# Kernel optimization log

Measured on AMD Instinct MI355X. Metric: run time of the kernel, lower is better.

The kernel has to match this reference:

```python
import jax, jax.numpy as jnp
import numpy as np

B, T, C, H, D = 8, 2048, 1024, 1024, 4  # batch, seq_len, input_size, hidden_size, dilation


def setup_inputs() -> dict:
    key = jax.random.key(0)
    k1, k2, k3, k4, k5 = jax.random.split(key, 5)
    s = 1.0 / np.sqrt(H).astype(np.float32)  # match nn.LSTM uniform(-1/sqrt(H),1/sqrt(H)) scale
    return {
        "x": jax.random.normal(k1, (B, T, C), jnp.float32),
        "W_ih": jax.random.normal(k2, (4 * H, C), jnp.float32) * s,
        "W_hh": jax.random.normal(k3, (4 * H, H), jnp.float32) * s,
        "b_ih": jax.random.normal(k4, (4 * H,), jnp.float32) * s,
        "b_hh": jax.random.normal(k5, (4 * H,), jnp.float32) * s,
    }


def _dilated_lstm(x, W_ih, W_hh, b_ih, b_hh):
    Bv, Tv, Cv = x.shape
    Tp = -(-Tv // D) * D          # ceil(T/D)*D, static
    L = Tp // D                   # sub-sequence length per dilation phase
    xp = jnp.pad(x, ((0, 0), (0, Tp - Tv), (0, 0)))
    # (B, L, D, C) -> (B, D, L, C) -> (B*D, L, C): D parallel strided slices
    xr = xp.reshape(Bv, L, D, Cv).transpose(0, 2, 1, 3).reshape(Bv * D, L, Cv)
    # Precompute input contribution to all gates once (big GEMM, hoisted out of scan)
    xg = jnp.einsum('blc,gc->blg', xr, W_ih) + b_ih + b_hh  # (B*D, L, 4H)

    h0 = jnp.zeros((Bv * D, H), x.dtype)
    c0 = jnp.zeros((Bv * D, H), x.dtype)

    def step(carry, g_t):
        h, c = carry
        g = g_t + h @ W_hh.T                    # (B*D, 4H), torch gate order i,f,g,o
        i, f, gg, o = jnp.split(g, 4, axis=-1)
        i = jax.nn.sigmoid(i)
        f = jax.nn.sigmoid(f)
        gg = jnp.tanh(gg)
        o = jax.nn.sigmoid(o)
        c = f * c + i * gg
        h = o * jnp.tanh(c)
        return (h, c), h

    _, ys = jax.lax.scan(step, (h0, c0), xg.transpose(1, 0, 2))  # ys: (L, B*D, H)
    y = ys.transpose(1, 0, 2)                                    # (B*D, L, H)
    y = y.reshape(Bv, D, L, H).transpose(0, 2, 1, 3).reshape(Bv, Tp, H)
    return y[:, :Tv, :]


def reference(x, W_ih, W_hh, b_ih, b_hh):
    return _dilated_lstm(x, W_ih, W_hh, b_ih, b_hh)
```

## Files before the change

### kernel.cpp

```cpp
#include <hip/hip_runtime.h>
#include <cstdint>

typedef __attribute__((ext_vector_type(8))) _Float16 half8;
typedef __attribute__((ext_vector_type(4))) _Float16 half4;
typedef __attribute__((ext_vector_type(4))) float f32x4;
typedef unsigned short u16;
typedef unsigned int u32;
typedef unsigned long long u64;

#define MFMA16F(a, b, c) __builtin_amdgcn_mfma_f32_16x16x32_f16((a), (b), (c), 0, 0, 0)
#define AGENT __HIP_MEMORY_SCOPE_AGENT

template <int AUX>
__device__ __forceinline__ void gl_lds16_a(const void* g, void* lds) {
  __builtin_amdgcn_global_load_lds(
      (const __attribute__((address_space(1))) unsigned*)g,
      (__attribute__((address_space(3))) unsigned*)lds, 16, 0, AUX);
}

__device__ __forceinline__ float sigm(float x) { return 1.f / (1.f + __expf(-x)); }
__device__ __forceinline__ float tanh_f(float x) { return 2.f / (1.f + __expf(-2.f * x)) - 1.f; }

__global__ void k_cvt(const float* __restrict__ in, _Float16* __restrict__ o, int n4) {
  int i = blockIdx.x * blockDim.x + threadIdx.x;
  int stride = gridDim.x * blockDim.x;
  for (; i < n4; i += stride) {
    float4 v = ((const float4*)in)[i];
    half4 h = {(_Float16)v.x, (_Float16)v.y, (_Float16)v.z, (_Float16)v.w};
    ((half4*)o)[i] = h;
  }
}

__global__ void k_bias(const float* __restrict__ bi, const float* __restrict__ bh,
                       float* __restrict__ bias) {
  int i = blockIdx.x * blockDim.x + threadIdx.x;
  if (i < 4096) bias[i] = bi[i] + bh[i];
}

__global__ void k_init4(u64* __restrict__ hf, u32* __restrict__ rdz) {
  const int i = blockIdx.x * blockDim.x + threadIdx.x;
  const u64 v = (i < 8192) ? 0ull : 0x0001000100010001ull;
  __hip_atomic_store(&hf[i], v, __ATOMIC_RELAXED, AGENT);
  if (i < 16) __hip_atomic_store(&rdz[i], 0u, __ATOMIC_RELAXED, AGENT);
}

__global__ __launch_bounds__(256) void k_gemm1(
    const u16* __restrict__ Aw, const u16* __restrict__ Bw,
    const float* __restrict__ bias, _Float16* __restrict__ xg) {
  __shared__ u16 sA[4096];
  __shared__ u16 sB[4096];
  const int tid = threadIdx.x, lane = tid & 63, wid = tid >> 6;
  const int bm = blockIdx.x >> 5, bn = blockIdx.x & 31;
  const int m0 = bm * 128, n0 = bn * 128;
  const int wr = wid >> 1, wc = wid & 1;
  f32x4 acc[4][4] = {};

  for (int kt = 0; kt < 32; ++kt) {
#pragma unroll
    for (int rb = 0; rb < 2; ++rb) {
      const int base = (rb * 4 + wid) * 1024;
      const int b = base + lane * 16;
      const int row = b >> 6;
      const int q = lane & 3;
      const int sq = ((q - row) & 3) << 4;
      gl_lds16_a<0>((const char*)Aw + (size_t)(m0 + row) * 2048 + (size_t)kt * 64 + sq,
                    (char*)&sA[0] + base);
      gl_lds16_a<0>((const char*)Bw + (size_t)(n0 + row) * 2048 + (size_t)kt * 64 + sq,
                    (char*)&sB[0] + base);
    }
    __syncthreads();
    half8 ah[4], bh[4];
#pragma unroll
    for (int i = 0; i < 4; ++i) {
      const int ra = wr * 64 + i * 16 + (lane & 15);
      ah[i] = *(const half8*)((const char*)sA + ra * 64 + ((((lane >> 4) + ra) & 3) << 4));
      const int rb2 = wc * 64 + i * 16 + (lane & 15);
      bh[i] = *(const half8*)((const char*)sB + rb2 * 64 + ((((lane >> 4) + rb2) & 3) << 4));
    }
#pragma unroll
    for (int i = 0; i < 4; ++i)
#pragma unroll
      for (int j = 0; j < 4; ++j) acc[i][j] = MFMA16F(ah[i], bh[j], acc[i][j]);
    __syncthreads();
  }

#pragma unroll
  for (int j = 0; j < 4; ++j) {
    const int gcol = n0 + wc * 64 + j * 16 + (lane & 15);
    const int gate = gcol >> 10, jj = gcol & 1023;
    const float bv = bias[gcol];
#pragma unroll
    for (int i = 0; i < 4; ++i)
#pragma unroll
      for (int q = 0; q < 4; ++q) {
        const int m = m0 + wr * 64 + i * 16 + (lane >> 4) * 4 + q;
        const int b = m >> 11, t = m & 2047;
        const int s = (b << 2) | (t & 3);
        const int l = t >> 2;
        xg[(((size_t)(l * 32 + s)) * 1024 + jj) * 4 + gate] = (_Float16)(acc[i][j][q] + bv);
      }
  }
}

__global__ __launch_bounds__(512, 1) void k_scan(
    const u16* __restrict__ Whh16, const _Float16* __restrict__ xg,
    u16* __restrict__ hfrag, float* __restrict__ out, u32* __restrict__ rdz) {
  const int b = blockIdx.x;
  const int tid = threadIdx.x;
  const int lane = tid & 63, wid = tid >> 6;

  __shared__ u16 h_lds[2][4096];
  __shared__ u32 sh_gr, sh_wl, sh_mode;

  if (tid == 0) {
    u32 my;
    asm volatile("s_getreg_b32 %0, hwreg(HW_REG_XCC_ID)" : "=s"(my));
    my &= 7u;
    const u32 rank = __hip_atomic_fetch_add(&rdz[my], 1u, __ATOMIC_RELAXED, AGENT);
    __hip_atomic_fetch_add(&rdz[8], 1u, __ATOMIC_RELAXED, AGENT);
    while (__hip_atomic_load(&rdz[8], __ATOMIC_RELAXED, AGENT) < 256u)
      __builtin_amdgcn_s_sleep(1);
    u32 okloc = 1;
    for (int x = 0; x < 8; ++x)
      okloc &= (__hip_atomic_load(&rdz[x], __ATOMIC_RELAXED, AGENT) == 32u);
    sh_gr = okloc ? my : (u32)(b >> 5);
    sh_wl = okloc ? rank : (u32)(b & 31);
    sh_mode = okloc ? 0u : 1u;
  }
  __syncthreads();
  const int gr = (int)sh_gr, wl = (int)sh_wl;
  int mode = (int)sh_mode;
  const int j0 = wl * 32;

  half8 wf[32];
  {
    const int p = lane & 15;
    const int gate = p >> 2, c = p & 3;
    const int koff = (lane >> 4) * 8;
    const size_t rowbase = (size_t)(gate * 1024 + j0 + wid * 4 + c) * 1024;
#pragma unroll
    for (int ks = 0; ks < 32; ++ks) {
      wf[ks] = *(const half8*)(Whh16 + rowbase + ks * 32 + koff);
      asm volatile("" : "+v"(wf[ks]));
    }
  }

  const int m = (lane >> 2) & 3;
  const int jl = (wid << 2) | (lane & 3);
  const int s = gr * 4 + m;
  const int j = j0 + jl;
  float c_reg = 0.f;
  const int hq = wl * 32 + m * 8 + wid;

  const u64 M = 0x0001000100010001ull;

  float x0 = 0.f, x1 = 0.f, x2 = 0.f, x3 = 0.f;
  if (lane < 16) {
    const half4 xv = *(const half4*)(xg + ((size_t)s * 1024 + j) * 4);
    x0 = (float)xv[0]; x1 = (float)xv[1]; x2 = (float)xv[2]; x3 = (float)xv[3];
  }

  for (int l = 0; l < 512; ++l) {
    const char* hsrc = (const char*)hfrag + (size_t)(l & 3) * 65536 + gr * 8192;
    u64* hdst = (u64*)((char*)hfrag + (size_t)((l + 1) & 3) * 65536 + gr * 8192);
    const u64 expv = ((l >> 2) & 1) ? M : 0ull;
    const u32 pw = (u32)(((l + 1) >> 2) & 1);
    u16* ldsb = &h_lds[l & 1][0];

    {
      int tries = 0;
      for (;;) {
        if (mode == 0)
          gl_lds16_a<1>(hsrc + wid * 1024 + lane * 16, (char*)ldsb + wid * 1024);
        else
          gl_lds16_a<17>(hsrc + wid * 1024 + lane * 16, (char*)ldsb + wid * 1024);
        asm volatile("s_waitcnt vmcnt(0)" ::: "memory");
        const u64* q = (const u64*)((const char*)ldsb + wid * 1024 + lane * 16);
        const bool ok = (((q[0] ^ expv) & M) == 0) & (((q[1] ^ expv) & M) == 0);
        if (__all(ok)) break;
        if (++tries > 64) mode = 1;
      }
    }
    __syncthreads();

    f32x4 a0 = {0.f, 0.f, 0.f, 0.f}, a1 = a0, a2 = a0, a3 = a0;
    const char* ab = (const char*)ldsb + (lane & 3) * 64 + (lane >> 4) * 16;
#pragma unroll
    for (int ks = 0; ks < 32; ks += 4) {
      const char* cb = ab + ks * 256;
      a0 = MFMA16F(*(const half8*)(cb), wf[ks], a0);
      a1 = MFMA16F(*(const half8*)(cb + 256), wf[ks + 1], a1);
      a2 = MFMA16F(*(const half8*)(cb + 512), wf[ks + 2], a2);
      a3 = MFMA16F(*(const half8*)(cb + 768), wf[ks + 3], a3);
    }
    float G0 = (a0[0] + a1[0]) + (a2[0] + a3[0]);
    float G1 = (a0[1] + a1[1]) + (a2[1] + a3[1]);
    float G2 = (a0[2] + a1[2]) + (a2[2] + a3[2]);
    float G3 = (a0[3] + a1[3]) + (a2[3] + a3[3]);

    {
      const bool h2 = (lane & 4) != 0;
      float x, y;
      x = h2 ? G0 : G1; y = __shfl_xor(x, 4);
      G0 = h2 ? y : G0; G1 = h2 ? G1 : y;
      x = h2 ? G2 : G3; y = __shfl_xor(x, 4);
      G2 = h2 ? y : G2; G3 = h2 ? G3 : y;
    }
    {
      const bool h3 = (lane & 8) != 0;
      float x, y;
      x = h3 ? G0 : G2; y = __shfl_xor(x, 8);
      G0 = h3 ? y : G0; G2 = h3 ? G2 : y;
      x = h3 ? G1 : G3; y = __shfl_xor(x, 8);
      G1 = h3 ? y : G1; G3 = h3 ? G3 : y;
    }

    const float gi = G0 + x0, gf = G1 + x1, gg = G2 + x2, go = G3 + x3;
    const float iv = sigm(gi), fv = sigm(gf), gv = tanh_f(gg), ov = sigm(go);
    c_reg = fv * c_reg + iv * gv;
    const float hv = ov * tanh_f(c_reg);

    if (lane < 16) {
      u32 hb = (u32)__builtin_bit_cast(u16, (_Float16)hv);
      hb = (hb & 0xFFFEu) | pw;
      const u32 o1 = (u32)__shfl_xor((int)hb, 1);
      const u32 w1 = (lane & 1) ? ((o1 & 0xFFFFu) | (hb << 16))
                                : ((hb & 0xFFFFu) | (o1 << 16));
      const u32 o2lo = (u32)__shfl_xor((int)w1, 2);
      const u64 v = (lane & 2) ? (((u64)w1 << 32) | (u64)o2lo)
                               : (((u64)o2lo << 32) | (u64)w1);
      if ((lane & 3) == 0)
        __hip_atomic_store(&hdst[hq], v, __ATOMIC_RELAXED, AGENT);

      out[(((size_t)(s >> 2) * 2048) + (size_t)l * 4 + (s & 3)) * 1024 + j] = hv;

      if (l < 511) {
        const half4 xv = *(const half4*)(xg + (((size_t)(l + 1) * 32 + s) * 1024 + j) * 4);
        x0 = (float)xv[0]; x1 = (float)xv[1]; x2 = (float)xv[2]; x3 = (float)xv[3];
      }
    }
  }
}

extern "C" void kernel_launch(void* const* d_in, const int* in_sizes, int n_in,
                              void* d_out, int out_size, void* d_ws, size_t ws_size,
                              hipStream_t stream) {
  const float* x   = (const float*)d_in[0];
  const float* Wih = (const float*)d_in[1];
  const float* Whh = (const float*)d_in[2];
  const float* bih = (const float*)d_in[3];
  const float* bhh = (const float*)d_in[4];
  float* out = (float*)d_out;
  char* ws = (char*)d_ws;

  constexpr size_t OFF_WIH16 = 0;
  constexpr size_t OFF_WHH16 = 8388608;
  constexpr size_t OFF_BIAS  = 16777216;
  constexpr size_t OFF_HFRAG = 16793600;
  constexpr size_t OFF_RDZ   = 17055744;
  constexpr size_t OFF_XG    = 17055808;
  constexpr size_t WS_NEED   = OFF_XG + 134217728;

  if (ws_size < WS_NEED) {
    hipMemsetAsync(d_out, 0, (size_t)out_size * sizeof(float), stream);
    return;
  }

  _Float16* wih16 = (_Float16*)(ws + OFF_WIH16);
  _Float16* whh16 = (_Float16*)(ws + OFF_WHH16);
  float* bias = (float*)(ws + OFF_BIAS);
  u16* hfrag = (u16*)(ws + OFF_HFRAG);
  u32* rdz = (u32*)(ws + OFF_RDZ);
  _Float16* xg = (_Float16*)(ws + OFF_XG);
  _Float16* x16 = (_Float16*)d_out;

  k_cvt<<<1024, 256, 0, stream>>>(Wih, wih16, 4194304 / 4);
  k_cvt<<<1024, 256, 0, stream>>>(Whh, whh16, 4194304 / 4);
  k_cvt<<<2048, 256, 0, stream>>>(x, x16, 16777216 / 4);
  k_bias<<<16, 256, 0, stream>>>(bih, bhh, bias);
  k_init4<<<128, 256, 0, stream>>>((u64*)hfrag, rdz);
  k_gemm1<<<4096, 256, 0, stream>>>((const u16*)x16, (const u16*)wih16, bias, xg);
  k_scan<<<256, 512, 0, stream>>>((const u16*)whh16, xg, hfrag, out, rdz);
}
```

Baseline: 1.272 ms.

## Swap MFMA operands to drop gate shuffles and add global rank rendezvous

The recurrent MFMA now takes the weight fragment as the A operand, so each lane's accumulator already holds all four gates for one (sequence, hidden) pair. This removes the cross-lane shuffles that regrouped gate values. The per-step xg load is issued before the barrier so it overlaps the MFMA work, and an s_sleep is added at the end of each step. Block-to-slot assignment now uses a prefix-sum rendezvous with a uniformity check of the XCC layout in place of the old all-XCC-equal test, which needs a larger rendezvous area and a shifted workspace offset. The added sleep could lengthen the latency-critical serial loop.

```diff
diff --git a/kernel.cpp b/kernel.cpp
--- a/kernel.cpp
+++ b/kernel.cpp
@@ -41,7 +41,7 @@
   const int i = blockIdx.x * blockDim.x + threadIdx.x;
   const u64 v = (i < 8192) ? 0ull : 0x0001000100010001ull;
   __hip_atomic_store(&hf[i], v, __ATOMIC_RELAXED, AGENT);
-  if (i < 16) __hip_atomic_store(&rdz[i], 0u, __ATOMIC_RELAXED, AGENT);
+  if (i < 272) __hip_atomic_store(&rdz[i], 0u, __ATOMIC_RELAXED, AGENT);
 }
 
 __global__ __launch_bounds__(256) void k_gemm1(
@@ -105,7 +105,6 @@
 __global__ __launch_bounds__(512, 1) void k_scan(
     const u16* __restrict__ Whh16, const _Float16* __restrict__ xg,
     u16* __restrict__ hfrag, float* __restrict__ out, u32* __restrict__ rdz) {
-  const int b = blockIdx.x;
   const int tid = threadIdx.x;
   const int lane = tid & 63, wid = tid >> 6;
 
@@ -117,15 +116,22 @@
     asm volatile("s_getreg_b32 %0, hwreg(HW_REG_XCC_ID)" : "=s"(my));
     my &= 7u;
     const u32 rank = __hip_atomic_fetch_add(&rdz[my], 1u, __ATOMIC_RELAXED, AGENT);
-    __hip_atomic_fetch_add(&rdz[8], 1u, __ATOMIC_RELAXED, AGENT);
-    while (__hip_atomic_load(&rdz[8], __ATOMIC_RELAXED, AGENT) < 256u)
+    __hip_atomic_fetch_add(&rdz[8], 1u, __ATOMIC_RELEASE, AGENT);
+    while (__hip_atomic_load(&rdz[8], __ATOMIC_ACQUIRE, AGENT) < 256u)
       __builtin_amdgcn_s_sleep(1);
-    u32 okloc = 1;
-    for (int x = 0; x < 8; ++x)
-      okloc &= (__hip_atomic_load(&rdz[x], __ATOMIC_RELAXED, AGENT) == 32u);
-    sh_gr = okloc ? my : (u32)(b >> 5);
-    sh_wl = okloc ? rank : (u32)(b & 31);
-    sh_mode = okloc ? 0u : 1u;
+    u32 prefix = 0;
+    for (u32 x = 0; x < my; ++x)
+      prefix += __hip_atomic_load(&rdz[x], __ATOMIC_RELAXED, AGENT);
+    const u32 g = prefix + rank;
+    __hip_atomic_store(&rdz[16 + g], my, __ATOMIC_RELAXED, AGENT);
+    __hip_atomic_fetch_add(&rdz[9], 1u, __ATOMIC_RELEASE, AGENT);
+    while (__hip_atomic_load(&rdz[9], __ATOMIC_ACQUIRE, AGENT) < 256u)
+      __builtin_amdgcn_s_sleep(1);
+    const u32 gr = g >> 5, wl = g & 31;
+    u32 uniform = 1;
+    for (int i = 0; i < 32; ++i)
+      uniform &= (__hip_atomic_load(&rdz[16 + gr * 32 + i], __ATOMIC_RELAXED, AGENT) == my);
+    sh_gr = gr; sh_wl = wl; sh_mode = uniform ? 0u : 1u;
   }
   __syncthreads();
   const int gr = (int)sh_gr, wl = (int)sh_wl;
@@ -135,7 +141,7 @@
   half8 wf[32];
   {
     const int p = lane & 15;
-    const int gate = p >> 2, c = p & 3;
+    const int gate = p & 3, c = p >> 2;
     const int koff = (lane >> 4) * 8;
     const size_t rowbase = (size_t)(gate * 1024 + j0 + wid * 4 + c) * 1024;
 #pragma unroll
@@ -145,8 +151,9 @@
     }
   }
 
-  const int m = (lane >> 2) & 3;
-  const int jl = (wid << 2) | (lane & 3);
+  const bool act = (lane & 12) == 0;
+  const int m = lane & 3;
+  const int jl = (wid << 2) | (lane >> 4);
   const int s = gr * 4 + m;
   const int j = j0 + jl;
   float c_reg = 0.f;
@@ -154,11 +161,8 @@
 
   const u64 M = 0x0001000100010001ull;
 
-  float x0 = 0.f, x1 = 0.f, x2 = 0.f, x3 = 0.f;
-  if (lane < 16) {
-    const half4 xv = *(const half4*)(xg + ((size_t)s * 1024 + j) * 4);
-    x0 = (float)xv[0]; x1 = (float)xv[1]; x2 = (float)xv[2]; x3 = (float)xv[3];
-  }
+  half4 xv_cur = {};
+  if (act) xv_cur = *(const half4*)(xg + ((size_t)s * 1024 + j) * 4);
 
   for (int l = 0; l < 512; ++l) {
     const char* hsrc = (const char*)hfrag + (size_t)(l & 3) * 65536 + gr * 8192;
@@ -181,6 +185,11 @@
         if (++tries > 64) mode = 1;
       }
     }
+
+    half4 xv_nxt = {};
+    if (act && l < 511)
+      xv_nxt = *(const half4*)(xg + (((size_t)(l + 1) * 32 + s) * 1024 + j) * 4);
+
     __syncthreads();
 
     f32x4 a0 = {0.f, 0.f, 0.f, 0.f}, a1 = a0, a2 = a0, a3 = a0;
@@ -188,57 +197,40 @@
 #pragma unroll
     for (int ks = 0; ks < 32; ks += 4) {
       const char* cb = ab + ks * 256;
-      a0 = MFMA16F(*(const half8*)(cb), wf[ks], a0);
-      a1 = MFMA16F(*(const half8*)(cb + 256), wf[ks + 1], a1);
-      a2 = MFMA16F(*(const half8*)(cb + 512), wf[ks + 2], a2);
-      a3 = MFMA16F(*(const half8*)(cb + 768), wf[ks + 3], a3);
-    }
-    float G0 = (a0[0] + a1[0]) + (a2[0] + a3[0]);
-    float G1 = (a0[1] + a1[1]) + (a2[1] + a3[1]);
-    float G2 = (a0[2] + a1[2]) + (a2[2] + a3[2]);
-    float G3 = (a0[3] + a1[3]) + (a2[3] + a3[3]);
-
-    {
-      const bool h2 = (lane & 4) != 0;
-      float x, y;
-      x = h2 ? G0 : G1; y = __shfl_xor(x, 4);
-      G0 = h2 ? y : G0; G1 = h2 ? G1 : y;
-      x = h2 ? G2 : G3; y = __shfl_xor(x, 4);
-      G2 = h2 ? y : G2; G3 = h2 ? G3 : y;
-    }
-    {
-      const bool h3 = (lane & 8) != 0;
-      float x, y;
-      x = h3 ? G0 : G2; y = __shfl_xor(x, 8);
-      G0 = h3 ? y : G0; G2 = h3 ? G2 : y;
-      x = h3 ? G1 : G3; y = __shfl_xor(x, 8);
-      G1 = h3 ? y : G1; G3 = h3 ? G3 : y;
-    }
-
-    const float gi = G0 + x0, gf = G1 + x1, gg = G2 + x2, go = G3 + x3;
+      a0 = MFMA16F(wf[ks], *(const half8*)(cb), a0);
+      a1 = MFMA16F(wf[ks + 1], *(const half8*)(cb + 256), a1);
+      a2 = MFMA16F(wf[ks + 2], *(const half8*)(cb + 512), a2);
+      a3 = MFMA16F(wf[ks + 3], *(const half8*)(cb + 768), a3);
+    }
+    const float G0 = (a0[0] + a1[0]) + (a2[0] + a3[0]);
+    const float G1 = (a0[1] + a1[1]) + (a2[1] + a3[1]);
+    const float G2 = (a0[2] + a1[2]) + (a2[2] + a3[2]);
+    const float G3 = (a0[3] + a1[3]) + (a2[3] + a3[3]);
+
+    const float gi = G0 + (float)xv_cur[0], gf = G1 + (float)xv_cur[1];
+    const float gg = G2 + (float)xv_cur[2], go = G3 + (float)xv_cur[3];
     const float iv = sigm(gi), fv = sigm(gf), gv = tanh_f(gg), ov = sigm(go);
     c_reg = fv * c_reg + iv * gv;
     const float hv = ov * tanh_f(c_reg);
 
-    if (lane < 16) {
+    {
       u32 hb = (u32)__builtin_bit_cast(u16, (_Float16)hv);
       hb = (hb & 0xFFFEu) | pw;
-      const u32 o1 = (u32)__shfl_xor((int)hb, 1);
-      const u32 w1 = (lane & 1) ? ((o1 & 0xFFFFu) | (hb << 16))
-                                : ((hb & 0xFFFFu) | (o1 << 16));
-      const u32 o2lo = (u32)__shfl_xor((int)w1, 2);
-      const u64 v = (lane & 2) ? (((u64)w1 << 32) | (u64)o2lo)
-                               : (((u64)o2lo << 32) | (u64)w1);
-      if ((lane & 3) == 0)
+      const u32 o1 = (u32)__shfl_xor((int)hb, 16);
+      const u32 w1 = (lane & 16) ? ((o1 & 0xFFFFu) | (hb << 16))
+                                 : ((hb & 0xFFFFu) | (o1 << 16));
+      const u32 o2lo = (u32)__shfl_xor((int)w1, 32);
+      const u64 v = (lane & 32) ? (((u64)w1 << 32) | (u64)o2lo)
+                                : (((u64)o2lo << 32) | (u64)w1);
+      if (lane < 4)
         __hip_atomic_store(&hdst[hq], v, __ATOMIC_RELAXED, AGENT);
-
+    }
+
+    if (act)
       out[(((size_t)(s >> 2) * 2048) + (size_t)l * 4 + (s & 3)) * 1024 + j] = hv;
 
-      if (l < 511) {
-        const half4 xv = *(const half4*)(xg + (((size_t)(l + 1) * 32 + s) * 1024 + j) * 4);
-        x0 = (float)xv[0]; x1 = (float)xv[1]; x2 = (float)xv[2]; x3 = (float)xv[3];
-      }
-    }
+    __builtin_amdgcn_s_sleep(4);
+    xv_cur = xv_nxt;
   }
 }
 
@@ -258,7 +250,7 @@
   constexpr size_t OFF_BIAS  = 16777216;
   constexpr size_t OFF_HFRAG = 16793600;
   constexpr size_t OFF_RDZ   = 17055744;
-  constexpr size_t OFF_XG    = 17055808;
+  constexpr size_t OFF_XG    = 17056832;
   constexpr size_t WS_NEED   = OFF_XG + 134217728;
 
   if (ws_size < WS_NEED) {
```

New measurement: 1.449 ms. 13.9% more time.
